# Kernel tuning notes

Measured on AMD Instinct MI355X. Metric: run time of the kernel, lower is better.

The kernel has to match this reference:

```python
import jax, jax.numpy as jnp
from jax import lax
import numpy as np

B = 131072   # batch
F = 512      # resnet18 pooled feature dim
D = 32       # latent_dim
T = 4        # pre-drawn rejection-sampling trials (accept always fires on trial 0 for d=32,k>=1)
H = 512      # MLP hidden
FS = 32      # MLP final_size
O = 7        # num_classes * action_length


def _normalize(x, eps=1e-12):
    # matches torch F.normalize: x / max(||x||, eps)
    n = jnp.linalg.norm(x, axis=-1, keepdims=True)
    return x / jnp.maximum(n, eps)


def setup_inputs() -> dict:
    key = jax.random.key(0)
    ks = jax.random.split(key, 16)
    s = 0.02
    return {
        "h": jax.random.normal(ks[0], (B, F), jnp.float32),
        "v": jax.random.normal(ks[1], (B, D), jnp.float32),
        "zu": jax.random.uniform(ks[2], (T, B), jnp.float32),
        "uu": jax.random.uniform(ks[3], (T, B), jnp.float32),
        "W_mu": jax.random.normal(ks[4], (F, D), jnp.float32) * s,
        "b_mu": jnp.zeros((D,), jnp.float32),
        "W_k": jax.random.normal(ks[5], (F, 1), jnp.float32) * s,
        "b_k": jnp.zeros((1,), jnp.float32),
        "W1": jax.random.normal(ks[6], (D, H), jnp.float32) * s,
        "b1": jnp.zeros((H,), jnp.float32),
        "W2": jax.random.normal(ks[7], (H, H), jnp.float32) * s,
        "b2": jnp.zeros((H,), jnp.float32),
        "W3": jax.random.normal(ks[8], (H, FS), jnp.float32) * s,
        "b3": jnp.zeros((FS,), jnp.float32),
        "W4": jax.random.normal(ks[9], (FS, O), jnp.float32) * s,
        "b4": jnp.zeros((O,), jnp.float32),
    }


def _sample_vmf_radial(k, zu, uu, d):
    """Vectorized accept-reject radial sampling. k:[B], zu/uu:[T,B] -> w:[B].
    First-accept semantics across the T pre-drawn trials (replaces the Python
    per-sample while loop; for this module the first trial always accepts)."""
    def step(carry, inp):
        w, done = carry
        z_raw, u = inp
        e = jnp.exp(-2.0 * k)
        z = z_raw * (1.0 - e) + e
        w_t = 1.0 - jnp.log(z) / k
        acc = jnp.log(u) <= (d - 3.0) * jnp.log(w_t) + k * w_t
        take = jnp.logical_and(acc, jnp.logical_not(done))
        return (jnp.where(take, w_t, w), jnp.logical_or(done, acc)), None
    (w, _), _ = lax.scan(step, (jnp.zeros_like(k), jnp.zeros(k.shape, bool)), (zu, uu))
    return w


def reference(h, v, zu, uu, W_mu, b_mu, W_k, b_k, W1, b1, W2, b2, W3, b3, W4, b4):
    # encode
    mu = _normalize(h @ W_mu + b_mu)                     # [B, D]
    kappa = jax.nn.softplus(h @ W_k + b_k) + 1.0         # [B, 1]
    # reparameterize
    k = kappa[:, 0]
    w = _sample_vmf_radial(k, zu, uu, float(D))          # [B]
    vn = _normalize(v)
    u_h = _normalize(vn - mu)
    z = vn - 2.0 * jnp.sum(vn * u_h, axis=-1, keepdims=True) * u_h  # Householder
    z = z * w[:, None]
    # MLP head
    x = jax.nn.relu(z @ W1 + b1)
    x = jax.nn.relu(x @ W2 + b2)
    x = jax.nn.relu(x @ W3 + b3)
    out = x @ W4 + b4                                    # [B, O]
    return (out, mu, kappa)
```

## Files before the change

kernel.cpp:

```cpp
#include <hip/hip_runtime.h>
#include <stdint.h>

#define B_N 131072

typedef float        float4_ __attribute__((ext_vector_type(4)));
typedef short        short8  __attribute__((ext_vector_type(8)));
typedef unsigned int uint4_  __attribute__((ext_vector_type(4)));

__device__ __forceinline__ unsigned short f2bf(float f) {
    unsigned int u = __float_as_uint(f);
    u += 0x7fffu + ((u >> 16) & 1u);
    return (unsigned short)(u >> 16);
}
__device__ __forceinline__ unsigned int pack2bf(float lo, float hi) {
    return (unsigned int)f2bf(lo) | ((unsigned int)f2bf(hi) << 16);
}

__global__ void aehr_prep(const float* __restrict__ Wmu, const float* __restrict__ Wk,
                          const float* __restrict__ W1, const float* __restrict__ W2,
                          const float* __restrict__ W3,
                          unsigned short* __restrict__ wct, unsigned short* __restrict__ w1t,
                          unsigned short* __restrict__ w2k, unsigned short* __restrict__ w3p) {
    int idx = blockIdx.x * 256 + threadIdx.x;
    if (idx < 48 * 512) {
        int n = idx >> 9, k = idx & 511;
        float v = 0.0f;
        if (n < 32) v = Wmu[k * 32 + n];
        else if (n == 32) v = Wk[k];
        wct[idx] = f2bf(v);
    } else if (idx < 48 * 512 + 512 * 32) {
        int j = idx - 48 * 512;
        int n = j >> 5, k = j & 31;
        w1t[j] = f2bf(W1[k * 512 + n]);
    } else if (idx < 48 * 512 + 512 * 32 + 512 * 512) {
        int j = idx - (48 * 512 + 512 * 32);
        int i = j & 7, t = j >> 3;
        int n = t & 511, gk = t >> 9;
        int g = gk & 3, ks = gk >> 2;
        int col = ks * 32 + ((i < 4) ? (4 * g + i) : (16 + 4 * g + (i - 4)));
        w2k[j] = f2bf(W2[col * 512 + n]);
    } else if (idx < 48 * 512 + 512 * 32 + 512 * 512 + 32 * 512) {
        int j = idx - (48 * 512 + 512 * 32 + 512 * 512);
        int n = j >> 9, slot = j & 511;
        int s = slot >> 5, q = slot & 31, g = (q >> 3) & 3, i = q & 7;
        int col = s * 32 + ((i < 4) ? (4 * g + i) : (16 + 4 * g + (i - 4)));
        w3p[j] = f2bf(W3[col * 32 + n]);
    }
}

__global__ __launch_bounds__(256, 4) void aehr_front(
    const float* __restrict__ h, const float* __restrict__ v,
    const float* __restrict__ zu, const float* __restrict__ uu,
    const float* __restrict__ bmu, const float* __restrict__ bk,
    const unsigned short* __restrict__ wct,
    float* __restrict__ out, unsigned short* __restrict__ zws)
{
    const int tid = threadIdx.x;
    const int wv = tid >> 6;
    const int ln = tid & 63;
    const int g = ln >> 4;
    const int c = ln & 15;
    const int rowA = blockIdx.x * 64 + wv * 16 + c;

    float4_ fz = {0.f, 0.f, 0.f, 0.f};
    float4_ acc0 = fz, acc1 = fz, acc2 = fz;
    const float* hrow = h + (size_t)rowA * 512 + g * 8;

    for (int ks = 0; ks < 16; ++ks) {
        float4_ a0 = *(const float4_*)(hrow + ks * 32);
        float4_ a1 = *(const float4_*)(hrow + ks * 32 + 4);
        short8 af;
        af[0] = (short)f2bf(a0[0]); af[1] = (short)f2bf(a0[1]);
        af[2] = (short)f2bf(a0[2]); af[3] = (short)f2bf(a0[3]);
        af[4] = (short)f2bf(a1[0]); af[5] = (short)f2bf(a1[1]);
        af[6] = (short)f2bf(a1[2]); af[7] = (short)f2bf(a1[3]);
        int kbase = ks * 32 + g * 8;
        short8 bf0 = *(const short8*)(wct + (c * 512 + kbase));
        short8 bf1 = *(const short8*)(wct + ((16 + c) * 512 + kbase));
        short8 bf2 = *(const short8*)(wct + ((32 + c) * 512 + kbase));
        acc0 = __builtin_amdgcn_mfma_f32_16x16x32_bf16(af, bf0, acc0, 0, 0, 0);
        acc1 = __builtin_amdgcn_mfma_f32_16x16x32_bf16(af, bf1, acc1, 0, 0, 0);
        acc2 = __builtin_amdgcn_mfma_f32_16x16x32_bf16(af, bf2, acc2, 0, 0, 0);
    }

    const float bm0 = bmu[c], bm1 = bmu[16 + c];
    const float bk0 = bk[0];

    #pragma unroll
    for (int r = 0; r < 4; ++r) {
        const int gm = blockIdx.x * 64 + wv * 16 + 4 * g + r;
        float m0 = acc0[r] + bm0;
        float m1 = acc1[r] + bm1;
        float s = m0 * m0 + m1 * m1;
        s += __shfl_xor(s, 1); s += __shfl_xor(s, 2);
        s += __shfl_xor(s, 4); s += __shfl_xor(s, 8);
        float nrm = fmaxf(sqrtf(s), 1e-12f);
        float mu0 = m0 / nrm, mu1 = m1 / nrm;
        out[(size_t)B_N * 7 + (size_t)gm * 32 + c] = mu0;
        out[(size_t)B_N * 7 + (size_t)gm * 32 + 16 + c] = mu1;

        float kraw = __shfl(acc2[r], g * 16) + bk0;
        float kap = fmaxf(kraw, 0.f) + __logf(1.0f + __expf(-fabsf(kraw))) + 1.0f;
        if (c == 0) out[(size_t)B_N * 39 + gm] = kap;

        float e = __expf(-2.0f * kap);
        float ome = 1.0f - e;
        float w = 0.0f;
        bool done = false;
        #pragma unroll
        for (int t = 0; t < 4; ++t) {
            float zr = zu[t * B_N + gm];
            float ur = uu[t * B_N + gm];
            float zt = zr * ome + e;
            float wt = 1.0f - __logf(zt) / kap;
            bool ac = (__logf(ur) <= 29.0f * __logf(wt) + kap * wt);
            if (ac && !done) w = wt;
            done = done || ac;
        }

        float v0 = v[(size_t)gm * 32 + c];
        float v1 = v[(size_t)gm * 32 + 16 + c];
        float sv = v0 * v0 + v1 * v1;
        sv += __shfl_xor(sv, 1); sv += __shfl_xor(sv, 2);
        sv += __shfl_xor(sv, 4); sv += __shfl_xor(sv, 8);
        float vn = fmaxf(sqrtf(sv), 1e-12f);
        float vn0 = v0 / vn, vn1 = v1 / vn;

        float u0 = vn0 - mu0, u1 = vn1 - mu1;
        float su = u0 * u0 + u1 * u1;
        su += __shfl_xor(su, 1); su += __shfl_xor(su, 2);
        su += __shfl_xor(su, 4); su += __shfl_xor(su, 8);
        float un = fmaxf(sqrtf(su), 1e-12f);
        float uh0 = u0 / un, uh1 = u1 / un;

        float dt = vn0 * uh0 + vn1 * uh1;
        dt += __shfl_xor(dt, 1); dt += __shfl_xor(dt, 2);
        dt += __shfl_xor(dt, 4); dt += __shfl_xor(dt, 8);

        float z0 = (vn0 - 2.0f * dt * uh0) * w;
        float z1 = (vn1 - 2.0f * dt * uh1) * w;
        zws[(size_t)gm * 32 + c] = f2bf(z0);
        zws[(size_t)gm * 32 + 16 + c] = f2bf(z1);
    }
}

__global__ __launch_bounds__(512, 2) void aehr_mlp(
    const unsigned short* __restrict__ zws,
    const unsigned short* __restrict__ w1t,
    const unsigned short* __restrict__ w2k,
    const unsigned short* __restrict__ w3p,
    const float* __restrict__ b1, const float* __restrict__ b2,
    const float* __restrict__ b3, const float* __restrict__ W4,
    const float* __restrict__ b4,
    float* __restrict__ out)
{
    __shared__ __attribute__((aligned(16))) char smem[67584];
    const int tid = threadIdx.x;
    const int wv = tid >> 6;
    const int ln = tid & 63;
    const int g = ln >> 4;
    const int c = ln & 15;
    const int swz = (c & 7) << 4;
    const size_t rowbase = (size_t)blockIdx.x * 64;
    const float4_ fz = {0.f, 0.f, 0.f, 0.f};

    {
        short8 zf[4];
        #pragma unroll
        for (int rt = 0; rt < 4; ++rt)
            zf[rt] = *(const short8*)(zws + (rowbase + rt * 16 + c) * 32 + g * 8);

        #pragma unroll
        for (int sl = 0; sl < 2; ++sl) {
            const int nb0 = wv * 64 + sl * 32;
            short8 w1f0 = *(const short8*)(w1t + (nb0 + c) * 32 + g * 8);
            short8 w1f1 = *(const short8*)(w1t + (nb0 + 16 + c) * 32 + g * 8);
            float4_ bv0 = *(const float4_*)(b1 + nb0 + 4 * g);
            float4_ bv1 = *(const float4_*)(b1 + nb0 + 16 + 4 * g);
            const int S = wv * 2 + sl;
            #pragma unroll
            for (int rt = 0; rt < 4; ++rt) {
                float4_ d0 = __builtin_amdgcn_mfma_f32_16x16x32_bf16(w1f0, zf[rt], fz, 0, 0, 0);
                float4_ d1 = __builtin_amdgcn_mfma_f32_16x16x32_bf16(w1f1, zf[rt], fz, 0, 0, 0);
                uint4_ u;
                u[0] = pack2bf(fmaxf(d0[0] + bv0[0], 0.f), fmaxf(d0[1] + bv0[1], 0.f));
                u[1] = pack2bf(fmaxf(d0[2] + bv0[2], 0.f), fmaxf(d0[3] + bv0[3], 0.f));
                u[2] = pack2bf(fmaxf(d1[0] + bv1[0], 0.f), fmaxf(d1[1] + bv1[1], 0.f));
                u[3] = pack2bf(fmaxf(d1[2] + bv1[2], 0.f), fmaxf(d1[3] + bv1[3], 0.f));
                const int row = rt * 16 + c;
                *(uint4_*)(smem + row * 1024 + ((S * 64 + g * 16) ^ swz)) = u;
            }
        }
    }
    __syncthreads();

    float4_ acc[4][4];
    #pragma unroll
    for (int rt = 0; rt < 4; ++rt)
        #pragma unroll
        for (int nt = 0; nt < 4; ++nt) acc[rt][nt] = fz;

    #pragma unroll 2
    for (int ks = 0; ks < 16; ++ks) {
        const unsigned short* wb = w2k + (size_t)(ks * 4 + g) * 512 * 8 + (wv * 64 + c) * 8;
        short8 a[4];
        #pragma unroll
        for (int nt = 0; nt < 4; ++nt)
            a[nt] = *(const short8*)(wb + nt * 128);
        #pragma unroll
        for (int rt = 0; rt < 4; ++rt) {
            short8 bfr = *(const short8*)(smem + (rt * 16 + c) * 1024 + ((ks * 64 + g * 16) ^ swz));
            #pragma unroll
            for (int nt = 0; nt < 4; ++nt)
                acc[rt][nt] = __builtin_amdgcn_mfma_f32_16x16x32_bf16(a[nt], bfr, acc[rt][nt], 0, 0, 0);
        }
    }

    float4_ x3acc[4][2];
    #pragma unroll
    for (int rt = 0; rt < 4; ++rt) { x3acc[rt][0] = fz; x3acc[rt][1] = fz; }
    {
        short8 w3f[2][2];
        #pragma unroll
        for (int S = 0; S < 2; ++S)
            #pragma unroll
            for (int n3 = 0; n3 < 2; ++n3)
                w3f[S][n3] = *(const short8*)(w3p + (n3 * 16 + c) * 512 + (wv * 2 + S) * 32 + g * 8);

        float4_ bv0 = *(const float4_*)(b2 + wv * 64 + 4 * g);
        float4_ bv1 = *(const float4_*)(b2 + wv * 64 + 16 + 4 * g);
        float4_ bv2 = *(const float4_*)(b2 + wv * 64 + 32 + 4 * g);
        float4_ bv3 = *(const float4_*)(b2 + wv * 64 + 48 + 4 * g);

        #pragma unroll
        for (int rt = 0; rt < 4; ++rt) {
            union { uint4_ u; short8 s; } x2a, x2b;
            x2a.u[0] = pack2bf(fmaxf(acc[rt][0][0] + bv0[0], 0.f), fmaxf(acc[rt][0][1] + bv0[1], 0.f));
            x2a.u[1] = pack2bf(fmaxf(acc[rt][0][2] + bv0[2], 0.f), fmaxf(acc[rt][0][3] + bv0[3], 0.f));
            x2a.u[2] = pack2bf(fmaxf(acc[rt][1][0] + bv1[0], 0.f), fmaxf(acc[rt][1][1] + bv1[1], 0.f));
            x2a.u[3] = pack2bf(fmaxf(acc[rt][1][2] + bv1[2], 0.f), fmaxf(acc[rt][1][3] + bv1[3], 0.f));
            x2b.u[0] = pack2bf(fmaxf(acc[rt][2][0] + bv2[0], 0.f), fmaxf(acc[rt][2][1] + bv2[1], 0.f));
            x2b.u[1] = pack2bf(fmaxf(acc[rt][2][2] + bv2[2], 0.f), fmaxf(acc[rt][2][3] + bv2[3], 0.f));
            x2b.u[2] = pack2bf(fmaxf(acc[rt][3][0] + bv3[0], 0.f), fmaxf(acc[rt][3][1] + bv3[1], 0.f));
            x2b.u[3] = pack2bf(fmaxf(acc[rt][3][2] + bv3[2], 0.f), fmaxf(acc[rt][3][3] + bv3[3], 0.f));
            #pragma unroll
            for (int n3 = 0; n3 < 2; ++n3) {
                x3acc[rt][n3] = __builtin_amdgcn_mfma_f32_16x16x32_bf16(w3f[0][n3], x2a.s, x3acc[rt][n3], 0, 0, 0);
                x3acc[rt][n3] = __builtin_amdgcn_mfma_f32_16x16x32_bf16(w3f[1][n3], x2b.s, x3acc[rt][n3], 0, 0, 0);
            }
        }
    }
    __syncthreads();

    float* red = (float*)smem;
    #pragma unroll
    for (int rt = 0; rt < 4; ++rt)
        #pragma unroll
        for (int t3 = 0; t3 < 2; ++t3)
            #pragma unroll
            for (int r = 0; r < 4; ++r)
                red[wv * 2112 + (rt * 16 + c) * 33 + t3 * 16 + 4 * g + r] = x3acc[rt][t3][r];
    __syncthreads();

    float sums[4];
    #pragma unroll
    for (int k = 0; k < 4; ++k) {
        int idx = tid + k * 512;
        int row = idx >> 5, n = idx & 31;
        float s_ = b3[n];
        #pragma unroll
        for (int w_ = 0; w_ < 8; ++w_) s_ += red[w_ * 2112 + row * 33 + n];
        sums[k] = fmaxf(s_, 0.0f);
    }
    __syncthreads();

    float* x3f = (float*)smem;
    #pragma unroll
    for (int k = 0; k < 4; ++k) {
        int idx = tid + k * 512;
        x3f[(idx >> 5) * 33 + (idx & 31)] = sums[k];
    }
    __syncthreads();

    {
        const int row = tid >> 3;
        const int o = tid & 7;
        if (o < 7) {
            const size_t gm = rowbase + row;
            float acc4 = b4[o];
            #pragma unroll
            for (int ci = 0; ci < 32; ++ci)
                acc4 += x3f[row * 33 + ci] * W4[ci * 7 + o];
            out[gm * 7 + o] = acc4;
        }
    }
}

extern "C" void kernel_launch(void* const* d_in, const int* in_sizes, int n_in,
                              void* d_out, int out_size, void* d_ws, size_t ws_size,
                              hipStream_t stream) {
    const float* h   = (const float*)d_in[0];
    const float* v   = (const float*)d_in[1];
    const float* zu  = (const float*)d_in[2];
    const float* uu  = (const float*)d_in[3];
    const float* Wmu = (const float*)d_in[4];
    const float* bmu = (const float*)d_in[5];
    const float* Wk  = (const float*)d_in[6];
    const float* bk  = (const float*)d_in[7];
    const float* W1  = (const float*)d_in[8];
    const float* b1  = (const float*)d_in[9];
    const float* W2  = (const float*)d_in[10];
    const float* b2  = (const float*)d_in[11];
    const float* W3  = (const float*)d_in[12];
    const float* b3  = (const float*)d_in[13];
    const float* W4  = (const float*)d_in[14];
    const float* b4  = (const float*)d_in[15];

    float* out = (float*)d_out;
    char* ws = (char*)d_ws;
    unsigned short* zws = (unsigned short*)ws;
    unsigned short* wct = (unsigned short*)(ws + 8388608);
    unsigned short* w1t = (unsigned short*)(ws + 8437760);
    unsigned short* w2k = (unsigned short*)(ws + 8470528);
    unsigned short* w3p = (unsigned short*)(ws + 8994816);

    aehr_prep<<<1248, 256, 0, stream>>>(Wmu, Wk, W1, W2, W3, wct, w1t, w2k, w3p);
    aehr_front<<<2048, 256, 0, stream>>>(h, v, zu, uu, bmu, bk, wct, out, zws);
    aehr_mlp<<<2048, 512, 0, stream>>>(zws, w1t, w2k, w3p, b1, b2, b3, W4, b4, out);
}
```

Baseline: 175.0 us.

## Halve MLP block to four waves, each computing 128 hidden columns

The MLP kernel now runs 256 threads (four waves) per 64-row block instead of eight waves. Each wave owns 128 output columns of layers 1 and 2, so every LDS activation fragment feeds twice as many MFMAs and the cross-wave layer-3 reduction touches four partials instead of eight. The cost is 32 fp32x4 accumulators per lane, which raises register pressure and lowers occupancy (launch bounds 256,1). Fewer waves are also left per CU to hide memory latency.

```diff
diff --git a/kernel.cpp b/kernel.cpp
--- a/kernel.cpp
+++ b/kernel.cpp
@@ -144,7 +144,7 @@
     }
 }
 
-__global__ __launch_bounds__(512, 2) void aehr_mlp(
+__global__ __launch_bounds__(256, 1) void aehr_mlp(
     const unsigned short* __restrict__ zws,
     const unsigned short* __restrict__ w1t,
     const unsigned short* __restrict__ w2k,
@@ -171,13 +171,13 @@
             zf[rt] = *(const short8*)(zws + (rowbase + rt * 16 + c) * 32 + g * 8);
 
         #pragma unroll
-        for (int sl = 0; sl < 2; ++sl) {
-            const int nb0 = wv * 64 + sl * 32;
+        for (int sl = 0; sl < 4; ++sl) {
+            const int nb0 = wv * 128 + sl * 32;
             short8 w1f0 = *(const short8*)(w1t + (nb0 + c) * 32 + g * 8);
             short8 w1f1 = *(const short8*)(w1t + (nb0 + 16 + c) * 32 + g * 8);
             float4_ bv0 = *(const float4_*)(b1 + nb0 + 4 * g);
             float4_ bv1 = *(const float4_*)(b1 + nb0 + 16 + 4 * g);
-            const int S = wv * 2 + sl;
+            const int S = wv * 4 + sl;
             #pragma unroll
             for (int rt = 0; rt < 4; ++rt) {
                 float4_ d0 = __builtin_amdgcn_mfma_f32_16x16x32_bf16(w1f0, zf[rt], fz, 0, 0, 0);
@@ -194,24 +194,24 @@
     }
     __syncthreads();
 
-    float4_ acc[4][4];
+    float4_ acc[4][8];
     #pragma unroll
     for (int rt = 0; rt < 4; ++rt)
         #pragma unroll
-        for (int nt = 0; nt < 4; ++nt) acc[rt][nt] = fz;
+        for (int nt = 0; nt < 8; ++nt) acc[rt][nt] = fz;
 
     #pragma unroll 2
     for (int ks = 0; ks < 16; ++ks) {
-        const unsigned short* wb = w2k + (size_t)(ks * 4 + g) * 512 * 8 + (wv * 64 + c) * 8;
-        short8 a[4];
-        #pragma unroll
-        for (int nt = 0; nt < 4; ++nt)
+        const unsigned short* wb = w2k + (size_t)(ks * 4 + g) * 512 * 8 + (wv * 128 + c) * 8;
+        short8 a[8];
+        #pragma unroll
+        for (int nt = 0; nt < 8; ++nt)
             a[nt] = *(const short8*)(wb + nt * 128);
         #pragma unroll
         for (int rt = 0; rt < 4; ++rt) {
             short8 bfr = *(const short8*)(smem + (rt * 16 + c) * 1024 + ((ks * 64 + g * 16) ^ swz));
             #pragma unroll
-            for (int nt = 0; nt < 4; ++nt)
+            for (int nt = 0; nt < 8; ++nt)
                 acc[rt][nt] = __builtin_amdgcn_mfma_f32_16x16x32_bf16(a[nt], bfr, acc[rt][nt], 0, 0, 0);
         }
     }
@@ -219,35 +219,23 @@
     float4_ x3acc[4][2];
     #pragma unroll
     for (int rt = 0; rt < 4; ++rt) { x3acc[rt][0] = fz; x3acc[rt][1] = fz; }
-    {
-        short8 w3f[2][2];
-        #pragma unroll
-        for (int S = 0; S < 2; ++S)
-            #pragma unroll
-            for (int n3 = 0; n3 < 2; ++n3)
-                w3f[S][n3] = *(const short8*)(w3p + (n3 * 16 + c) * 512 + (wv * 2 + S) * 32 + g * 8);
-
-        float4_ bv0 = *(const float4_*)(b2 + wv * 64 + 4 * g);
-        float4_ bv1 = *(const float4_*)(b2 + wv * 64 + 16 + 4 * g);
-        float4_ bv2 = *(const float4_*)(b2 + wv * 64 + 32 + 4 * g);
-        float4_ bv3 = *(const float4_*)(b2 + wv * 64 + 48 + 4 * g);
-
+
+    #pragma unroll
+    for (int p = 0; p < 4; ++p) {
+        const int S2 = wv * 4 + p;
+        short8 w3f0 = *(const short8*)(w3p + c * 512 + S2 * 32 + g * 8);
+        short8 w3f1 = *(const short8*)(w3p + (16 + c) * 512 + S2 * 32 + g * 8);
+        float4_ bv0 = *(const float4_*)(b2 + wv * 128 + p * 32 + 4 * g);
+        float4_ bv1 = *(const float4_*)(b2 + wv * 128 + p * 32 + 16 + 4 * g);
         #pragma unroll
         for (int rt = 0; rt < 4; ++rt) {
-            union { uint4_ u; short8 s; } x2a, x2b;
-            x2a.u[0] = pack2bf(fmaxf(acc[rt][0][0] + bv0[0], 0.f), fmaxf(acc[rt][0][1] + bv0[1], 0.f));
-            x2a.u[1] = pack2bf(fmaxf(acc[rt][0][2] + bv0[2], 0.f), fmaxf(acc[rt][0][3] + bv0[3], 0.f));
-            x2a.u[2] = pack2bf(fmaxf(acc[rt][1][0] + bv1[0], 0.f), fmaxf(acc[rt][1][1] + bv1[1], 0.f));
-            x2a.u[3] = pack2bf(fmaxf(acc[rt][1][2] + bv1[2], 0.f), fmaxf(acc[rt][1][3] + bv1[3], 0.f));
-            x2b.u[0] = pack2bf(fmaxf(acc[rt][2][0] + bv2[0], 0.f), fmaxf(acc[rt][2][1] + bv2[1], 0.f));
-            x2b.u[1] = pack2bf(fmaxf(acc[rt][2][2] + bv2[2], 0.f), fmaxf(acc[rt][2][3] + bv2[3], 0.f));
-            x2b.u[2] = pack2bf(fmaxf(acc[rt][3][0] + bv3[0], 0.f), fmaxf(acc[rt][3][1] + bv3[1], 0.f));
-            x2b.u[3] = pack2bf(fmaxf(acc[rt][3][2] + bv3[2], 0.f), fmaxf(acc[rt][3][3] + bv3[3], 0.f));
-            #pragma unroll
-            for (int n3 = 0; n3 < 2; ++n3) {
-                x3acc[rt][n3] = __builtin_amdgcn_mfma_f32_16x16x32_bf16(w3f[0][n3], x2a.s, x3acc[rt][n3], 0, 0, 0);
-                x3acc[rt][n3] = __builtin_amdgcn_mfma_f32_16x16x32_bf16(w3f[1][n3], x2b.s, x3acc[rt][n3], 0, 0, 0);
-            }
+            union { uint4_ u; short8 s; } x2;
+            x2.u[0] = pack2bf(fmaxf(acc[rt][2*p][0] + bv0[0], 0.f), fmaxf(acc[rt][2*p][1] + bv0[1], 0.f));
+            x2.u[1] = pack2bf(fmaxf(acc[rt][2*p][2] + bv0[2], 0.f), fmaxf(acc[rt][2*p][3] + bv0[3], 0.f));
+            x2.u[2] = pack2bf(fmaxf(acc[rt][2*p+1][0] + bv1[0], 0.f), fmaxf(acc[rt][2*p+1][1] + bv1[1], 0.f));
+            x2.u[3] = pack2bf(fmaxf(acc[rt][2*p+1][2] + bv1[2], 0.f), fmaxf(acc[rt][2*p+1][3] + bv1[3], 0.f));
+            x3acc[rt][0] = __builtin_amdgcn_mfma_f32_16x16x32_bf16(w3f0, x2.s, x3acc[rt][0], 0, 0, 0);
+            x3acc[rt][1] = __builtin_amdgcn_mfma_f32_16x16x32_bf16(w3f1, x2.s, x3acc[rt][1], 0, 0, 0);
         }
     }
     __syncthreads();
@@ -262,28 +250,29 @@
                 red[wv * 2112 + (rt * 16 + c) * 33 + t3 * 16 + 4 * g + r] = x3acc[rt][t3][r];
     __syncthreads();
 
-    float sums[4];
-    #pragma unroll
-    for (int k = 0; k < 4; ++k) {
-        int idx = tid + k * 512;
+    float sums[8];
+    #pragma unroll
+    for (int k = 0; k < 8; ++k) {
+        int idx = tid + k * 256;
         int row = idx >> 5, n = idx & 31;
         float s_ = b3[n];
         #pragma unroll
-        for (int w_ = 0; w_ < 8; ++w_) s_ += red[w_ * 2112 + row * 33 + n];
+        for (int w_ = 0; w_ < 4; ++w_) s_ += red[w_ * 2112 + row * 33 + n];
         sums[k] = fmaxf(s_, 0.0f);
     }
     __syncthreads();
 
     float* x3f = (float*)smem;
     #pragma unroll
-    for (int k = 0; k < 4; ++k) {
-        int idx = tid + k * 512;
+    for (int k = 0; k < 8; ++k) {
+        int idx = tid + k * 256;
         x3f[(idx >> 5) * 33 + (idx & 31)] = sums[k];
     }
     __syncthreads();
 
-    {
-        const int row = tid >> 3;
+    #pragma unroll
+    for (int half = 0; half < 2; ++half) {
+        const int row = (tid >> 3) + half * 32;
         const int o = tid & 7;
         if (o < 7) {
             const size_t gm = rowbase + row;
@@ -326,5 +315,5 @@
 
     aehr_prep<<<1248, 256, 0, stream>>>(Wmu, Wk, W1, W2, W3, wct, w1t, w2k, w3p);
     aehr_front<<<2048, 256, 0, stream>>>(h, v, zu, uu, bmu, bk, wct, out, zws);
-    aehr_mlp<<<2048, 512, 0, stream>>>(zws, w1t, w2k, w3p, b1, b2, b3, W4, b4, out);
-}
+    aehr_mlp<<<2048, 256, 0, stream>>>(zws, w1t, w2k, w3p, b1, b2, b3, W4, b4, out);
+}
```

Result: slower. 206.1 us (+17.8%).
